# Kernel tuning notes

Measured on AMD Instinct MI355X. Metric: run time of the kernel, lower is better.

## Reference

```python
import jax, jax.numpy as jnp
import numpy as np

B, T, E, H, V = 64, 160, 512, 1024, 32000


def setup_inputs() -> dict:
    key = jax.random.key(0)
    ks = jax.random.split(key, 8)
    s = 1.0 / np.sqrt(H).astype(np.float32)
    return {
        "contexts": jax.random.randint(ks[0], (B, T), 0, V),
        "responses": jax.random.randint(ks[1], (B, T), 0, V),
        "emb": jax.random.normal(ks[2], (V, E), jnp.float32) * 0.02,
        "Wih": jax.random.uniform(ks[3], (4 * H, E), jnp.float32, -s, s),
        "Whh": jax.random.uniform(ks[4], (4 * H, H), jnp.float32, -s, s),
        "bih": jax.random.uniform(ks[5], (4 * H,), jnp.float32, -s, s),
        "bhh": jax.random.uniform(ks[6], (4 * H,), jnp.float32, -s, s),
        "M": jax.random.normal(ks[7], (H, H), jnp.float32),
    }


def _lstm_final_h(tokens, emb, Wih, Whh, bih, bhh):
    """Single-layer LSTM (PyTorch gate order i,f,g,o); returns final hidden state [B,H]."""
    x = emb[tokens]                      # [B, T, E]
    b = bih + bhh                        # [4H]
    hdim = Whh.shape[1]

    def step(carry, xt):
        h, c = carry
        gates = xt @ Wih.T + h @ Whh.T + b          # [B, 4H]
        i, f, g, o = jnp.split(gates, 4, axis=-1)
        c = jax.nn.sigmoid(f) * c + jax.nn.sigmoid(i) * jnp.tanh(g)
        h = jax.nn.sigmoid(o) * jnp.tanh(c)
        return (h, c), None

    h0 = jnp.zeros((tokens.shape[0], hdim), x.dtype)
    (h, _), _ = jax.lax.scan(step, (h0, h0), jnp.swapaxes(x, 0, 1))  # scan over time
    return h


def reference(contexts, responses, emb, Wih, Whh, bih, bhh, M):
    ch = _lstm_final_h(contexts, emb, Wih, Whh, bih, bhh)   # [B, H]
    rh = _lstm_final_h(responses, emb, Wih, Whh, bih, bhh)  # [B, H]
    # batched bilinear: sigmoid(diag(C @ M @ R^T)) -- replaces the per-example Python loop
    return jax.nn.sigmoid(jnp.einsum('bi,ij,bj->b', ch, M, rh))
```

## Files before the change

kernel.cpp:

```cpp
#include <hip/hip_runtime.h>
#include <math.h>


#define BB 64
#define TT 160
#define EE 512
#define HH 1024
#define G4 4096
#define ROWS 128
#define NBLK 64

typedef unsigned short u16;
typedef unsigned int u32;
typedef __attribute__((ext_vector_type(8))) __bf16 bf16x8;
typedef __attribute__((ext_vector_type(8))) short short8;
typedef __attribute__((ext_vector_type(4))) short short4v;
typedef __attribute__((ext_vector_type(4))) float f32x4;
typedef __attribute__((ext_vector_type(4))) u32 u32x4;
typedef __attribute__((ext_vector_type(2))) u32 u32x2;

__device__ __forceinline__ u16 f2b(float f) {
    unsigned u = __float_as_uint(f);
    u = u + 0x7fffu + ((u >> 16) & 1u);
    return (u16)(u >> 16);
}
__device__ __forceinline__ float b2f(u16 s) { return __uint_as_float(((unsigned)s) << 16); }

__device__ __forceinline__ f32x4 mfma16(short8 a, short8 b, f32x4 c) {
    return __builtin_amdgcn_mfma_f32_16x16x32_bf16(
        __builtin_bit_cast(bf16x8, a), __builtin_bit_cast(bf16x8, b), c, 0, 0, 0);
}

__device__ __forceinline__ void g2l16(const void* gsrc, void* ldst) {
    __builtin_amdgcn_global_load_lds(
        (const __attribute__((address_space(1))) u32*)gsrc,
        (__attribute__((address_space(3))) u32*)ldst, 16, 0, 0);
}
__device__ __forceinline__ void g2l16c(const void* gsrc, void* ldst) {
    __builtin_amdgcn_global_load_lds(
        (const __attribute__((address_space(1))) u32*)gsrc,
        (__attribute__((address_space(3))) u32*)ldst, 16, 0, 17);
}

__global__ __launch_bounds__(256) void cvt_kernel(const float* __restrict__ in,
                                                  u16* __restrict__ out, int n4) {
    int i = blockIdx.x * 256 + threadIdx.x;
    if (i < n4) {
        f32x4 v = *(const f32x4*)(in + (size_t)i * 4);
        short4v o;
        o.x = (short)f2b(v.x); o.y = (short)f2b(v.y);
        o.z = (short)f2b(v.z); o.w = (short)f2b(v.w);
        *(short4v*)(out + (size_t)i * 4) = o;
    }
}

__global__ __launch_bounds__(256) void pre_gemm2(
    const int* __restrict__ ctx, const int* __restrict__ rsp,
    const u16* __restrict__ embb, const u16* __restrict__ Wihb,
    const float* __restrict__ bih, const float* __restrict__ bhh,
    u16* __restrict__ xg)
{
    __shared__ __align__(16) u16 As[2][128][64];
    __shared__ __align__(16) u16 Ws[2][128][64];
    __shared__ int toks[128];
    const int tid = threadIdx.x;
    const int n0 = blockIdx.x * 128;
    const int t  = blockIdx.y;

    if (tid < 128) {
        int r = tid;
        toks[tid] = (r < BB) ? ctx[r * TT + t] : rsp[(r - BB) * TT + t];
    }
    __syncthreads();

    const u16* asrc[4]; const u16* bsrc[4];
    #pragma unroll
    for (int q = 0; q < 4; ++q) {
        int i = tid + q * 256;
        int row = i >> 3, c16 = i & 7;
        int scol = ((c16 ^ (row & 7)) * 8);
        asrc[q] = embb + (size_t)toks[row] * EE + scol;
        bsrc[q] = Wihb + (size_t)(n0 + row) * EE + scol;
    }

    const int lane = tid & 63, wave = tid >> 6;
    const int wr = (wave >> 1) * 64, wc = (wave & 1) * 64;
    const int l15 = lane & 15, l4 = lane >> 4;
    f32x4 acc[4][4] = {};

    #pragma unroll
    for (int q = 0; q < 4; ++q) {
        g2l16(asrc[q], (char*)&As[0][0][0] + (tid + q * 256) * 16);
        g2l16(bsrc[q], (char*)&Ws[0][0][0] + (tid + q * 256) * 16);
    }
    for (int it = 0; it < 8; ++it) {
        __syncthreads();
        if (it + 1 < 8) {
            int kk = (it + 1) * 64, bs = (it + 1) & 1;
            #pragma unroll
            for (int q = 0; q < 4; ++q) {
                g2l16(asrc[q] + kk, (char*)&As[bs][0][0] + (tid + q * 256) * 16);
                g2l16(bsrc[q] + kk, (char*)&Ws[bs][0][0] + (tid + q * 256) * 16);
            }
        }
        const int b = it & 1;
        #pragma unroll
        for (int ks = 0; ks < 2; ++ks) {
            int c16 = ks * 4 + l4;
            short8 a[4], w[4];
            #pragma unroll
            for (int mf = 0; mf < 4; ++mf) {
                int R = wr + mf * 16 + l15;
                a[mf] = *(const short8*)((const char*)&As[b][0][0] + R * 128 + ((c16 ^ (R & 7)) << 4));
            }
            #pragma unroll
            for (int nf = 0; nf < 4; ++nf) {
                int Nn = wc + nf * 16 + l15;
                w[nf] = *(const short8*)((const char*)&Ws[b][0][0] + Nn * 128 + ((c16 ^ (Nn & 7)) << 4));
            }
            #pragma unroll
            for (int mf = 0; mf < 4; ++mf)
                #pragma unroll
                for (int nf = 0; nf < 4; ++nf)
                    acc[mf][nf] = mfma16(a[mf], w[nf], acc[mf][nf]);
        }
    }

    u16* xp = xg + (size_t)t * ROWS * G4;
    #pragma unroll
    for (int nf = 0; nf < 4; ++nf) {
        int n = n0 + wc + nf * 16 + l15;
        float bias = bih[n] + bhh[n];
        #pragma unroll
        for (int mf = 0; mf < 4; ++mf)
            #pragma unroll
            for (int q = 0; q < 4; ++q) {
                int r = wr + mf * 16 + l4 * 4 + q;
                xp[(size_t)r * G4 + n] = f2b(acc[mf][nf][q] + bias);
            }
    }
}

__global__ __launch_bounds__(512, 2) void lstm_persist4(
    const u16* __restrict__ Whhb, const u16* __restrict__ xg,
    u16* __restrict__ hbuf, u32* __restrict__ flags)
{
    __shared__ __align__(16) u16 Abuf[64][512];
    __shared__ __align__(16) float G[2][64][132];

    const int tid = threadIdx.x;
    const int bx = blockIdx.x;
    const int cg = bx & 31, rg = bx >> 5;
    const int r0 = rg * 64, j0 = cg * 32;
    const int lane = tid & 63, w = tid >> 6;
    const int colt = w >> 2, q = w & 3;
    const int l15 = lane & 15, l4 = lane >> 4;

    short8 breg[4][8];
    #pragma unroll
    for (int nt = 0; nt < 4; ++nt) {
        int n = (colt * 2 + (nt >> 1)) * 1024 + j0 + (nt & 1) * 16 + l15;
        const u16* wp = Whhb + (size_t)n * HH + l4 * 8;
        #pragma unroll
        for (int z = 0; z < 8; ++z) {
            int kc = (z < 4) ? (q * 4 + z) : (16 + q * 4 + (z - 4));
            breg[nt][z] = *(const short8*)(wp + kc * 32);
        }
    }

    const int urow = tid >> 3;
    const int jj4  = (tid & 7) * 4;
    float cst[4] = {0.f, 0.f, 0.f, 0.f};

    __syncthreads();

    for (int t = 0; t < TT; ++t) {
        const u16* hin = hbuf + (size_t)(t & 1) * ROWS * HH;
        u16* hout      = hbuf + (size_t)((t + 1) & 1) * ROWS * HH;

        #pragma unroll
        for (int j = 0; j < 8; ++j) {
            int row = w * 8 + j;
            const u16* src = hin + (size_t)(r0 + row) * HH + ((lane ^ j) * 8);
            g2l16c(src, &Abuf[row][0]);
        }
        u32x2 xv[4];
        {
            const u16* xp = xg + ((size_t)t * ROWS + r0 + urow) * G4 + j0 + jj4;
            #pragma unroll
            for (int g = 0; g < 4; ++g)
                asm volatile("global_load_dwordx2 %0, %1, off"
                             : "=v"(xv[g]) : "v"(xp + g * HH));
        }

        f32x4 acc[4][4] = {};

        asm volatile("s_waitcnt vmcnt(4)" ::: "memory");
        __builtin_amdgcn_sched_barrier(0);
        __builtin_amdgcn_s_barrier();
        __builtin_amdgcn_sched_barrier(0);
        #pragma unroll
        for (int z4 = 0; z4 < 4; ++z4) {
            const int kcl = q * 4 + z4;
            short8 a[4];
            #pragma unroll
            for (int rt = 0; rt < 4; ++rt) {
                int row = rt * 16 + l15;
                int c16 = kcl * 4 + l4;
                a[rt] = *(const short8*)((const char*)&Abuf[0][0] +
                         row * 1024 + ((c16 ^ (l15 & 7)) << 4));
            }
            #pragma unroll
            for (int rt = 0; rt < 4; ++rt)
                #pragma unroll
                for (int nt = 0; nt < 4; ++nt)
                    acc[rt][nt] = mfma16(a[rt], breg[nt][z4], acc[rt][nt]);
        }
        asm volatile("s_waitcnt lgkmcnt(0)" ::: "memory");
        __builtin_amdgcn_s_barrier();
        __builtin_amdgcn_sched_barrier(0);

        #pragma unroll
        for (int j = 0; j < 8; ++j) {
            int row = w * 8 + j;
            const u16* src = hin + (size_t)(r0 + row) * HH + 512 + ((lane ^ j) * 8);
            g2l16c(src, &Abuf[row][0]);
        }
        asm volatile("s_waitcnt vmcnt(0)" ::: "memory");
        __builtin_amdgcn_sched_barrier(0);
        __builtin_amdgcn_s_barrier();
        __builtin_amdgcn_sched_barrier(0);
        #pragma unroll
        for (int z4 = 0; z4 < 4; ++z4) {
            const int kcl = q * 4 + z4;
            short8 a[4];
            #pragma unroll
            for (int rt = 0; rt < 4; ++rt) {
                int row = rt * 16 + l15;
                int c16 = kcl * 4 + l4;
                a[rt] = *(const short8*)((const char*)&Abuf[0][0] +
                         row * 1024 + ((c16 ^ (l15 & 7)) << 4));
            }
            #pragma unroll
            for (int rt = 0; rt < 4; ++rt)
                #pragma unroll
                for (int nt = 0; nt < 4; ++nt)
                    acc[rt][nt] = mfma16(a[rt], breg[nt][4 + z4], acc[rt][nt]);
        }

        if (q < 2) {
            #pragma unroll
            for (int rt = 0; rt < 4; ++rt)
                #pragma unroll
                for (int nt = 0; nt < 4; ++nt) {
                    int col = colt * 64 + nt * 16 + l15;
                    int rowb = rt * 16 + l4 * 4;
                    #pragma unroll
                    for (int e = 0; e < 4; ++e)
                        G[q][rowb + e][col] = acc[rt][nt][e];
                }
        }
        asm volatile("s_waitcnt lgkmcnt(0)" ::: "memory");
        __builtin_amdgcn_s_barrier();
        __builtin_amdgcn_sched_barrier(0);
        if (q >= 2) {
            #pragma unroll
            for (int rt = 0; rt < 4; ++rt)
                #pragma unroll
                for (int nt = 0; nt < 4; ++nt) {
                    int col = colt * 64 + nt * 16 + l15;
                    int rowb = rt * 16 + l4 * 4;
                    #pragma unroll
                    for (int e = 0; e < 4; ++e)
                        G[q - 2][rowb + e][col] += acc[rt][nt][e];
                }
        }
        asm volatile("s_waitcnt lgkmcnt(0)" ::: "memory");
        __builtin_amdgcn_s_barrier();
        __builtin_amdgcn_sched_barrier(0);

        float gv[4][4];
        #pragma unroll
        for (int g = 0; g < 4; ++g) {
            f32x4 a0 = *(const f32x4*)&G[0][urow][g * 32 + jj4];
            f32x4 a1 = *(const f32x4*)&G[1][urow][g * 32 + jj4];
            gv[g][0] = a0.x + a1.x + b2f((u16)(xv[g].x & 0xffffu));
            gv[g][1] = a0.y + a1.y + b2f((u16)(xv[g].x >> 16));
            gv[g][2] = a0.z + a1.z + b2f((u16)(xv[g].y & 0xffffu));
            gv[g][3] = a0.w + a1.w + b2f((u16)(xv[g].y >> 16));
        }
        u16 hp[4];
        #pragma unroll
        for (int e = 0; e < 4; ++e) {
            float ii = 1.f / (1.f + expf(-gv[0][e]));
            float ff = 1.f / (1.f + expf(-gv[1][e]));
            float gg = tanhf(gv[2][e]);
            float oo = 1.f / (1.f + expf(-gv[3][e]));
            cst[e] = ff * cst[e] + ii * gg;
            hp[e] = f2b(oo * tanhf(cst[e]));
        }
        u32x2 hw;
        hw.x = (u32)hp[0] | ((u32)hp[1] << 16);
        hw.y = (u32)hp[2] | ((u32)hp[3] << 16);
        {
            u16* hpt = hout + (size_t)(r0 + urow) * HH + j0 + jj4;
            asm volatile("global_store_dwordx2 %0, %1, off sc0 sc1"
                         :: "v"(hpt), "v"(hw) : "memory");
        }

        if (t < TT - 1) {
            asm volatile("s_waitcnt vmcnt(0)" ::: "memory");
            __builtin_amdgcn_s_barrier();
            __builtin_amdgcn_sched_barrier(0);
            const u32 target = (u32)(t + 1);
            if (tid == 0)
                asm volatile("global_store_dword %0, %1, off sc0 sc1"
                             :: "v"(flags + bx), "v"(target) : "memory");
            if (w == 0) {
                const u32* fp = flags + rg * 32 + (lane & 7) * 4;
                int spins = 0;
                while (true) {
                    u32x4 fv;
                    asm volatile("global_load_dwordx4 %0, %1, off sc0 sc1"
                                 : "=v"(fv) : "v"(fp));
                    asm volatile("s_waitcnt vmcnt(0)" ::: "memory");
                    bool ok = (fv.x >= target) & (fv.y >= target) &
                              (fv.z >= target) & (fv.w >= target);
                    if (__all(ok)) break;
                    __builtin_amdgcn_s_sleep(2);
                    if (++spins > 2000000) break;
                }
            }
            __builtin_amdgcn_s_barrier();
            __builtin_amdgcn_sched_barrier(0);
        }
    }
}

template<int MODE>
__global__ __launch_bounds__(256) void step_fused(
    const int* __restrict__ ctx, const int* __restrict__ rsp,
    const u16* __restrict__ embb, const u16* __restrict__ Wihb,
    const u16* __restrict__ Whhb, const u16* __restrict__ xg,
    const float* __restrict__ bih, const float* __restrict__ bhh,
    const u16* __restrict__ hin, u16* __restrict__ hout,
    float* __restrict__ c_ws, int t)
{
    __shared__ __align__(16) u16 As[2][64][64];
    __shared__ __align__(16) u16 Ws[2][32][64];
    __shared__ float gs[64][32];
    __shared__ int toks[64];

    const int tid = threadIdx.x;
    const int cg = blockIdx.x & 127, rg = blockIdx.x >> 7;
    const int r0 = rg * 64, j0 = cg * 8;

    if (MODE == 1) {
        if (tid < 64) {
            int r = r0 + tid;
            toks[tid] = (r < BB) ? ctx[r * TT + t] : rsp[(r - BB) * TT + t];
        }
        __syncthreads();
    }

    const int arow0 = tid >> 3, c16a = tid & 7;
    const int arow1 = arow0 + 32;
    const int acol0 = ((c16a ^ (arow0 & 7)) * 8);
    const int acol1 = ((c16a ^ (arow1 & 7)) * 8);
    const u16* hA0 = hin + (size_t)(r0 + arow0) * HH + acol0;
    const u16* hA1 = hin + (size_t)(r0 + arow1) * HH + acol1;
    const u16* eA0 = nullptr; const u16* eA1 = nullptr;
    if (MODE == 1) {
        eA0 = embb + (size_t)toks[arow0] * EE + acol0;
        eA1 = embb + (size_t)toks[arow1] * EE + acol1;
    }
    const int nn = tid >> 3, c16b = tid & 7;
    const int bcol = ((c16b ^ (nn & 7)) * 8);
    const int wrow = (nn >> 3) * HH + j0 + (nn & 7);
    const u16* wHh = Whhb + (size_t)wrow * HH + bcol;
    const u16* wIh = (MODE == 1) ? (Wihb + (size_t)wrow * EE + bcol) : nullptr;

    const int NK = (MODE == 1) ? 24 : 16;

    auto stage = [&](int bs, int it) {
        int kk = it * 64;
        const u16 *s0, *s1, *sw;
        if (MODE == 1 && kk < EE) {
            s0 = eA0 + kk; s1 = eA1 + kk; sw = wIh + kk;
        } else {
            int khh = (MODE == 1) ? kk - EE : kk;
            s0 = hA0 + khh; s1 = hA1 + khh; sw = wHh + khh;
        }
        g2l16(s0, (char*)&As[bs][0][0] + tid * 16);
        g2l16(s1, (char*)&As[bs][0][0] + (tid + 256) * 16);
        g2l16(sw, (char*)&Ws[bs][0][0] + tid * 16);
    };

    const int lane = tid & 63, wave = tid >> 6;
    const int wr = wave * 16;
    const int l15 = lane & 15, l4 = lane >> 4;
    f32x4 acc[2] = {};

    stage(0, 0);
    for (int it = 0; it < NK; ++it) {
        __syncthreads();
        if (it + 1 < NK) stage((it + 1) & 1, it + 1);
        const int b = it & 1;
        #pragma unroll
        for (int ks = 0; ks < 2; ++ks) {
            int c16 = ks * 4 + l4;
            int R = wr + l15;
            short8 a = *(const short8*)((const char*)&As[b][0][0] + R * 128 + ((c16 ^ (R & 7)) << 4));
            #pragma unroll
            for (int nf = 0; nf < 2; ++nf) {
                int Nn = nf * 16 + l15;
                short8 w = *(const short8*)((const char*)&Ws[b][0][0] + Nn * 128 + ((c16 ^ (Nn & 7)) << 4));
                acc[nf] = mfma16(a, w, acc[nf]);
            }
        }
    }
    __syncthreads();
    #pragma unroll
    for (int nf = 0; nf < 2; ++nf)
        #pragma unroll
        for (int q = 0; q < 4; ++q)
            gs[wr + l4 * 4 + q][nf * 16 + l15] = acc[nf][q];
    __syncthreads();

    const int e = tid * 2;
    const int row = e >> 3, jj = e & 7;
    const int rglob = r0 + row;
    float g0[4], g1[4];
    #pragma unroll
    for (int g = 0; g < 4; ++g) { g0[g] = gs[row][g * 8 + jj]; g1[g] = gs[row][g * 8 + jj + 1]; }
    if (MODE == 2) {
        const u16* xp = xg + ((size_t)t * ROWS + rglob) * G4 + j0 + jj;
        #pragma unroll
        for (int g = 0; g < 4; ++g) { g0[g] += b2f(xp[g * HH]); g1[g] += b2f(xp[g * HH + 1]); }
    } else {
        #pragma unroll
        for (int g = 0; g < 4; ++g) {
            int n = g * HH + j0 + jj;
            g0[g] += bih[n] + bhh[n];
            g1[g] += bih[n + 1] + bhh[n + 1];
        }
    }
    size_t cidx = ((size_t)blockIdx.x * 64 + row) * 8 + jj;
    float c0 = c_ws[cidx], c1 = c_ws[cidx + 1];
    float i0 = 1.f / (1.f + expf(-g0[0])), i1 = 1.f / (1.f + expf(-g1[0]));
    float f0 = 1.f / (1.f + expf(-g0[1])), f1 = 1.f / (1.f + expf(-g1[1]));
    float t0 = tanhf(g0[2]),               t1 = tanhf(g1[2]);
    float o0 = 1.f / (1.f + expf(-g0[3])), o1 = 1.f / (1.f + expf(-g1[3]));
    float cn0 = f0 * c0 + i0 * t0;
    float cn1 = f1 * c1 + i1 * t1;
    c_ws[cidx] = cn0; c_ws[cidx + 1] = cn1;
    float h0 = o0 * tanhf(cn0), h1 = o1 * tanhf(cn1);
    unsigned hpk = (unsigned)f2b(h0) | ((unsigned)f2b(h1) << 16);
    *(unsigned*)(hout + (size_t)rglob * HH + j0 + jj) = hpk;
}

__global__ __launch_bounds__(256) void step_gemm_f32(
    const int* __restrict__ ctx, const int* __restrict__ rsp,
    const float* __restrict__ emb, const float* __restrict__ Wih, const float* __restrict__ Whh,
    const u16* __restrict__ hb, float* __restrict__ gates, int t)
{
    __shared__ __align__(16) u16 As[64][32];
    __shared__ __align__(16) u16 Ws[64][32];
    __shared__ int toks[64];
    const int tid = threadIdx.x;
    const int n0 = blockIdx.x * 64;
    const int r0 = blockIdx.y * 64;
    const int part = blockIdx.z;
    if (tid < 64) {
        int r = r0 + tid;
        toks[tid] = (r < BB) ? ctx[r * TT + t] : rsp[(r - BB) * TT + t];
    }
    __syncthreads();
    const int lane = tid & 63, wave = tid >> 6;
    const int wr = (wave >> 1) * 32, wc = (wave & 1) * 32;
    const int l15 = lane & 15, l4 = lane >> 4;
    f32x4 acc[2][2] = {};
    const int kstart = part * 768;
    const int srow = tid >> 2;
    const int sseg = (tid & 3) * 8;
    for (int it = 0; it < 24; ++it) {
        const int kg = kstart + it * 32;
        const int kk = kg + sseg;
        if (kg < EE) {
            const float* s = emb + (size_t)toks[srow] * EE + kk;
            #pragma unroll
            for (int q = 0; q < 8; ++q) As[srow][sseg + q] = f2b(s[q]);
            const float* sw = Wih + (size_t)(n0 + srow) * EE + kk;
            #pragma unroll
            for (int q = 0; q < 8; ++q) Ws[srow][sseg + q] = f2b(sw[q]);
        } else {
            *(short8*)&As[srow][sseg] = *(const short8*)(hb + (size_t)(r0 + srow) * HH + (kk - EE));
            const float* sw = Whh + (size_t)(n0 + srow) * HH + (kk - EE);
            #pragma unroll
            for (int q = 0; q < 8; ++q) Ws[srow][sseg + q] = f2b(sw[q]);
        }
        __syncthreads();
        #pragma unroll
        for (int mf = 0; mf < 2; ++mf)
            #pragma unroll
            for (int nf = 0; nf < 2; ++nf)
                acc[mf][nf] = mfma16(*(const short8*)&As[wr + mf * 16 + l15][l4 * 8],
                                     *(const short8*)&Ws[wc + nf * 16 + l15][l4 * 8], acc[mf][nf]);
        __syncthreads();
    }
    float* gp = gates + (size_t)part * ROWS * G4;
    #pragma unroll
    for (int mf = 0; mf < 2; ++mf)
        #pragma unroll
        for (int nf = 0; nf < 2; ++nf)
            #pragma unroll
            for (int q = 0; q < 4; ++q) {
                int r = r0 + wr + mf * 16 + l4 * 4 + q;
                int n = n0 + wc + nf * 16 + l15;
                gp[(size_t)r * G4 + n] = acc[mf][nf][q];
            }
}

__global__ __launch_bounds__(256) void lstm_update0(
    const float* __restrict__ gates, const float* __restrict__ bih, const float* __restrict__ bhh,
    u16* __restrict__ hb, float* __restrict__ c)
{
    int idx = blockIdx.x * 256 + threadIdx.x;
    int r = idx >> 8;
    int jj = (idx & 255) * 4;
    const float* gp0 = gates + (size_t)r * G4;
    const float* gp1 = gates + (size_t)(ROWS + r) * G4;
    float gate[4][4];
    #pragma unroll
    for (int g = 0; g < 4; ++g) {
        int n = g * HH + jj;
        f32x4 a = *(const f32x4*)(gp0 + n);
        f32x4 b = *(const f32x4*)(gp1 + n);
        #pragma unroll
        for (int q = 0; q < 4; ++q) gate[g][q] = a[q] + b[q] + bih[n + q] + bhh[n + q];
    }
    int cidx = r * HH + jj;
    f32x4 cv = *(const f32x4*)(c + cidx);
    f32x4 cn; short4v hn;
    #pragma unroll
    for (int q = 0; q < 4; ++q) {
        float si = 1.f / (1.f + expf(-gate[0][q]));
        float sf = 1.f / (1.f + expf(-gate[1][q]));
        float tg = tanhf(gate[2][q]);
        float so = 1.f / (1.f + expf(-gate[3][q]));
        float cval = sf * cv[q] + si * tg;
        cn[q] = cval;
        ((short*)&hn)[q] = (short)f2b(so * tanhf(cval));
    }
    *(f32x4*)(c + cidx) = cn;
    *(short4v*)(hb + cidx) = hn;
}

__global__ __launch_bounds__(256) void bilinear(
    const u16* __restrict__ hb, const float* __restrict__ M, float* __restrict__ out)
{
    int b = blockIdx.x;
    __shared__ float chs[HH];
    __shared__ float red[256];
    const u16* ch = hb + (size_t)b * HH;
    const u16* rh = hb + (size_t)(BB + b) * HH;
    for (int i = threadIdx.x; i < HH; i += 256) chs[i] = b2f(ch[i]);
    __syncthreads();
    float vj[4] = {0.f, 0.f, 0.f, 0.f};
    for (int i = 0; i < HH; ++i) {
        float chi = chs[i];
        const float* Mr = M + (size_t)i * HH;
        #pragma unroll
        for (int q = 0; q < 4; ++q) vj[q] += chi * Mr[threadIdx.x + q * 256];
    }
    float acc = 0.f;
    #pragma unroll
    for (int q = 0; q < 4; ++q) acc += vj[q] * b2f(rh[threadIdx.x + q * 256]);
    red[threadIdx.x] = acc;
    __syncthreads();
    for (int s = 128; s > 0; s >>= 1) {
        if (threadIdx.x < s) red[threadIdx.x] += red[threadIdx.x + s];
        __syncthreads();
    }
    if (threadIdx.x == 0) out[b] = 1.0f / (1.0f + expf(-red[0]));
}

extern "C" void kernel_launch(void* const* d_in, const int* in_sizes, int n_in,
                              void* d_out, int out_size, void* d_ws, size_t ws_size,
                              hipStream_t stream) {
    const int*   ctx = (const int*)d_in[0];
    const int*   rsp = (const int*)d_in[1];
    const float* emb = (const float*)d_in[2];
    const float* Wih = (const float*)d_in[3];
    const float* Whh = (const float*)d_in[4];
    const float* bih = (const float*)d_in[5];
    const float* bhh = (const float*)d_in[6];
    const float* M   = (const float*)d_in[7];
    float* out = (float*)d_out;

    char* w = (char*)d_ws;
    u16*   hbuf  = (u16*)w;   w += (size_t)2 * ROWS * HH * 2;
    float* c_ws  = (float*)w; w += (size_t)ROWS * HH * 4;
    float* gates = (float*)w; w += (size_t)2 * ROWS * G4 * 4;
    u16*   embb  = (u16*)w;   w += (size_t)32000 * EE * 2;
    u16*   Wihb  = (u16*)w;   w += (size_t)G4 * EE * 2;
    u16*   Whhb  = (u16*)w;   w += (size_t)G4 * HH * 2;
    u32*   flags = (u32*)w;   w += 1024;
    size_t conv_need = (size_t)(w - (char*)d_ws);
    u16*   xg    = (u16*)w;   w += (size_t)TT * ROWS * G4 * 2;
    size_t xpre_need = (size_t)(w - (char*)d_ws);

    int mode = (ws_size >= xpre_need) ? 2 : (ws_size >= conv_need) ? 1 : 0;

    hipMemsetAsync(hbuf, 0, (size_t)2 * ROWS * HH * 2, stream);

    if (mode >= 1) {
        cvt_kernel<<<16000, 256, 0, stream>>>(emb, embb, 32000 * EE / 4);
        cvt_kernel<<<2048,  256, 0, stream>>>(Wih, Wihb, G4 * EE / 4);
        cvt_kernel<<<4096,  256, 0, stream>>>(Whh, Whhb, G4 * HH / 4);
    }

    if (mode == 2) {
        hipMemsetAsync(flags, 0, 1024, stream);
        pre_gemm2<<<dim3(G4 / 128, TT), 256, 0, stream>>>(ctx, rsp, embb, Wihb, bih, bhh, xg);
        lstm_persist4<<<NBLK, 512, 0, stream>>>(Whhb, xg, hbuf, flags);
        bilinear<<<BB, 256, 0, stream>>>(hbuf, M, out);
    } else if (mode == 1) {
        hipMemsetAsync(c_ws, 0, (size_t)ROWS * HH * 4, stream);
        for (int t = 0; t < TT; ++t) {
            const u16* hin = hbuf + (size_t)(t & 1) * ROWS * HH;
            u16* hout      = hbuf + (size_t)((t + 1) & 1) * ROWS * HH;
            step_fused<1><<<256, 256, 0, stream>>>(ctx, rsp, embb, Wihb, Whhb, xg,
                                                   bih, bhh, hin, hout, c_ws, t);
        }
        bilinear<<<BB, 256, 0, stream>>>(hbuf, M, out);
    } else {
        hipMemsetAsync(c_ws, 0, (size_t)ROWS * HH * 4, stream);
        u16* hb = hbuf;
        dim3 sg(G4 / 64, ROWS / 64, 2);
        for (int t = 0; t < TT; ++t) {
            step_gemm_f32<<<sg, 256, 0, stream>>>(ctx, rsp, emb, Wih, Whh, hb, gates, t);
            lstm_update0<<<128, 256, 0, stream>>>(gates, bih, bhh, hb, c_ws);
        }
        bilinear<<<BB, 256, 0, stream>>>(hb, M, out);
    }
}
```

Measured before the change: 2.005 ms.

## Load full hidden row into double LDS buffer, pad barrier flags, use fast activations

The persistent LSTM kernel now loads both halves of the hidden state into two LDS buffers in one pass and runs the full K loop without the mid-step reload and barrier. The gate-reduction buffer is aliased onto that LDS, which keeps shared memory near its old size. The inter-block flags are spread to one per 128-byte line, and the spin loop reads single dwords with a shorter sleep, to cut contention in the cross-block barrier. Sigmoid and tanh switch to exp2/rcp intrinsics, which lowers transcendental cost at a small accuracy risk.

```diff
diff --git a/kernel.cpp b/kernel.cpp
--- a/kernel.cpp
+++ b/kernel.cpp
@@ -16,7 +16,6 @@
 typedef __attribute__((ext_vector_type(8))) short short8;
 typedef __attribute__((ext_vector_type(4))) short short4v;
 typedef __attribute__((ext_vector_type(4))) float f32x4;
-typedef __attribute__((ext_vector_type(4))) u32 u32x4;
 typedef __attribute__((ext_vector_type(2))) u32 u32x2;
 
 __device__ __forceinline__ u16 f2b(float f) {
@@ -25,6 +24,14 @@
     return (u16)(u >> 16);
 }
 __device__ __forceinline__ float b2f(u16 s) { return __uint_as_float(((unsigned)s) << 16); }
+
+#define LOG2E 1.4426950408889634f
+__device__ __forceinline__ float sigf(float x) {
+    return __builtin_amdgcn_rcpf(1.f + __builtin_amdgcn_exp2f(-LOG2E * x));
+}
+__device__ __forceinline__ float tanhf_fast(float x) {
+    return 1.f - 2.f * __builtin_amdgcn_rcpf(1.f + __builtin_amdgcn_exp2f(2.f * LOG2E * x));
+}
 
 __device__ __forceinline__ f32x4 mfma16(short8 a, short8 b, f32x4 c) {
     return __builtin_amdgcn_mfma_f32_16x16x32_bf16(
@@ -141,12 +148,11 @@
     }
 }
 
-__global__ __launch_bounds__(512, 2) void lstm_persist4(
+__global__ __launch_bounds__(512, 2) void lstm_persist7(
     const u16* __restrict__ Whhb, const u16* __restrict__ xg,
-    u16* __restrict__ hbuf, u32* __restrict__ flags)
+    u16* __restrict__ hbuf, u32* __restrict__ barr)
 {
-    __shared__ __align__(16) u16 Abuf[64][512];
-    __shared__ __align__(16) float G[2][64][132];
+    __shared__ __align__(16) u16 Abuf[2][64][512];
 
     const int tid = threadIdx.x;
     const int bx = blockIdx.x;
@@ -156,6 +162,8 @@
     const int colt = w >> 2, q = w & 3;
     const int l15 = lane & 15, l4 = lane >> 4;
 
+    float* const G = (float*)&Abuf[0][0][0];
+
     short8 breg[4][8];
     #pragma unroll
     for (int nt = 0; nt < 4; ++nt) {
@@ -172,6 +180,8 @@
     const int jj4  = (tid & 7) * 4;
     float cst[4] = {0.f, 0.f, 0.f, 0.f};
 
+    u32* const cb = barr + (size_t)rg * 2048;
+
     __syncthreads();
 
     for (int t = 0; t < TT; ++t) {
@@ -181,8 +191,9 @@
         #pragma unroll
         for (int j = 0; j < 8; ++j) {
             int row = w * 8 + j;
-            const u16* src = hin + (size_t)(r0 + row) * HH + ((lane ^ j) * 8);
-            g2l16c(src, &Abuf[row][0]);
+            const u16* src = hin + (size_t)(r0 + row) * HH + ((lane ^ (row & 7)) * 8);
+            g2l16c(src,       &Abuf[0][row][0]);
+            g2l16c(src + 512, &Abuf[1][row][0]);
         }
         u32x2 xv[4];
         {
@@ -200,53 +211,28 @@
         __builtin_amdgcn_s_barrier();
         __builtin_amdgcn_sched_barrier(0);
         #pragma unroll
-        for (int z4 = 0; z4 < 4; ++z4) {
-            const int kcl = q * 4 + z4;
-            short8 a[4];
-            #pragma unroll
-            for (int rt = 0; rt < 4; ++rt) {
-                int row = rt * 16 + l15;
-                int c16 = kcl * 4 + l4;
-                a[rt] = *(const short8*)((const char*)&Abuf[0][0] +
-                         row * 1024 + ((c16 ^ (l15 & 7)) << 4));
-            }
-            #pragma unroll
-            for (int rt = 0; rt < 4; ++rt)
+        for (int half = 0; half < 2; ++half) {
+            #pragma unroll
+            for (int z4 = 0; z4 < 4; ++z4) {
+                const int kcl = q * 4 + z4;
+                short8 a[4];
                 #pragma unroll
-                for (int nt = 0; nt < 4; ++nt)
-                    acc[rt][nt] = mfma16(a[rt], breg[nt][z4], acc[rt][nt]);
+                for (int rt = 0; rt < 4; ++rt) {
+                    int row = rt * 16 + l15;
+                    int c16 = kcl * 4 + l4;
+                    a[rt] = *(const short8*)((const char*)&Abuf[half][0][0] +
+                             row * 1024 + ((c16 ^ (l15 & 7)) << 4));
+                }
+                #pragma unroll
+                for (int rt = 0; rt < 4; ++rt)
+                    #pragma unroll
+                    for (int nt = 0; nt < 4; ++nt)
+                        acc[rt][nt] = mfma16(a[rt], breg[nt][half * 4 + z4], acc[rt][nt]);
+            }
         }
         asm volatile("s_waitcnt lgkmcnt(0)" ::: "memory");
         __builtin_amdgcn_s_barrier();
         __builtin_amdgcn_sched_barrier(0);
-
-        #pragma unroll
-        for (int j = 0; j < 8; ++j) {
-            int row = w * 8 + j;
-            const u16* src = hin + (size_t)(r0 + row) * HH + 512 + ((lane ^ j) * 8);
-            g2l16c(src, &Abuf[row][0]);
-        }
-        asm volatile("s_waitcnt vmcnt(0)" ::: "memory");
-        __builtin_amdgcn_sched_barrier(0);
-        __builtin_amdgcn_s_barrier();
-        __builtin_amdgcn_sched_barrier(0);
-        #pragma unroll
-        for (int z4 = 0; z4 < 4; ++z4) {
-            const int kcl = q * 4 + z4;
-            short8 a[4];
-            #pragma unroll
-            for (int rt = 0; rt < 4; ++rt) {
-                int row = rt * 16 + l15;
-                int c16 = kcl * 4 + l4;
-                a[rt] = *(const short8*)((const char*)&Abuf[0][0] +
-                         row * 1024 + ((c16 ^ (l15 & 7)) << 4));
-            }
-            #pragma unroll
-            for (int rt = 0; rt < 4; ++rt)
-                #pragma unroll
-                for (int nt = 0; nt < 4; ++nt)
-                    acc[rt][nt] = mfma16(a[rt], breg[nt][4 + z4], acc[rt][nt]);
-        }
 
         if (q < 2) {
             #pragma unroll
@@ -257,7 +243,7 @@
                     int rowb = rt * 16 + l4 * 4;
                     #pragma unroll
                     for (int e = 0; e < 4; ++e)
-                        G[q][rowb + e][col] = acc[rt][nt][e];
+                        G[((size_t)q * 64 + rowb + e) * 132 + col] = acc[rt][nt][e];
                 }
         }
         asm volatile("s_waitcnt lgkmcnt(0)" ::: "memory");
@@ -272,18 +258,21 @@
                     int rowb = rt * 16 + l4 * 4;
                     #pragma unroll
                     for (int e = 0; e < 4; ++e)
-                        G[q - 2][rowb + e][col] += acc[rt][nt][e];
+                        G[((size_t)(q - 2) * 64 + rowb + e) * 132 + col] += acc[rt][nt][e];
                 }
         }
         asm volatile("s_waitcnt lgkmcnt(0)" ::: "memory");
         __builtin_amdgcn_s_barrier();
         __builtin_amdgcn_sched_barrier(0);
 
+        asm volatile("s_waitcnt vmcnt(0)" ::: "memory");
         float gv[4][4];
         #pragma unroll
         for (int g = 0; g < 4; ++g) {
-            f32x4 a0 = *(const f32x4*)&G[0][urow][g * 32 + jj4];
-            f32x4 a1 = *(const f32x4*)&G[1][urow][g * 32 + jj4];
+            const float* Gr0 = &G[((size_t)0 * 64 + urow) * 132 + g * 32 + jj4];
+            const float* Gr1 = &G[((size_t)1 * 64 + urow) * 132 + g * 32 + jj4];
+            f32x4 a0 = *(const f32x4*)Gr0;
+            f32x4 a1 = *(const f32x4*)Gr1;
             gv[g][0] = a0.x + a1.x + b2f((u16)(xv[g].x & 0xffffu));
             gv[g][1] = a0.y + a1.y + b2f((u16)(xv[g].x >> 16));
             gv[g][2] = a0.z + a1.z + b2f((u16)(xv[g].y & 0xffffu));
@@ -292,12 +281,12 @@
         u16 hp[4];
         #pragma unroll
         for (int e = 0; e < 4; ++e) {
-            float ii = 1.f / (1.f + expf(-gv[0][e]));
-            float ff = 1.f / (1.f + expf(-gv[1][e]));
-            float gg = tanhf(gv[2][e]);
-            float oo = 1.f / (1.f + expf(-gv[3][e]));
+            float ii = sigf(gv[0][e]);
+            float ff = sigf(gv[1][e]);
+            float gg = tanhf_fast(gv[2][e]);
+            float oo = sigf(gv[3][e]);
             cst[e] = ff * cst[e] + ii * gg;
-            hp[e] = f2b(oo * tanhf(cst[e]));
+            hp[e] = f2b(oo * tanhf_fast(cst[e]));
         }
         u32x2 hw;
         hw.x = (u32)hp[0] | ((u32)hp[1] << 16);
@@ -315,19 +304,17 @@
             const u32 target = (u32)(t + 1);
             if (tid == 0)
                 asm volatile("global_store_dword %0, %1, off sc0 sc1"
-                             :: "v"(flags + bx), "v"(target) : "memory");
+                             :: "v"(cb + cg * 32), "v"(target) : "memory");
             if (w == 0) {
-                const u32* fp = flags + rg * 32 + (lane & 7) * 4;
+                const u32* fp = cb + (lane & 31) * 32;
                 int spins = 0;
                 while (true) {
-                    u32x4 fv;
-                    asm volatile("global_load_dwordx4 %0, %1, off sc0 sc1"
-                                 : "=v"(fv) : "v"(fp));
+                    u32 v;
+                    asm volatile("global_load_dword %0, %1, off sc0 sc1"
+                                 : "=v"(v) : "v"(fp));
                     asm volatile("s_waitcnt vmcnt(0)" ::: "memory");
-                    bool ok = (fv.x >= target) & (fv.y >= target) &
-                              (fv.z >= target) & (fv.w >= target);
-                    if (__all(ok)) break;
-                    __builtin_amdgcn_s_sleep(2);
+                    if (__all(v >= target)) break;
+                    __builtin_amdgcn_s_sleep(1);
                     if (++spins > 2000000) break;
                 }
             }
@@ -605,7 +592,7 @@
     u16*   embb  = (u16*)w;   w += (size_t)32000 * EE * 2;
     u16*   Wihb  = (u16*)w;   w += (size_t)G4 * EE * 2;
     u16*   Whhb  = (u16*)w;   w += (size_t)G4 * HH * 2;
-    u32*   flags = (u32*)w;   w += 1024;
+    u32*   barr  = (u32*)w;   w += 16384;
     size_t conv_need = (size_t)(w - (char*)d_ws);
     u16*   xg    = (u16*)w;   w += (size_t)TT * ROWS * G4 * 2;
     size_t xpre_need = (size_t)(w - (char*)d_ws);
@@ -621,9 +608,9 @@
     }
 
     if (mode == 2) {
-        hipMemsetAsync(flags, 0, 1024, stream);
+        hipMemsetAsync(barr, 0, 16384, stream);
         pre_gemm2<<<dim3(G4 / 128, TT), 256, 0, stream>>>(ctx, rsp, embb, Wihb, bih, bhh, xg);
-        lstm_persist4<<<NBLK, 512, 0, stream>>>(Whhb, xg, hbuf, flags);
+        lstm_persist7<<<NBLK, 512, 0, stream>>>(Whhb, xg, hbuf, barr);
         bilinear<<<BB, 256, 0, stream>>>(hbuf, M, out);
     } else if (mode == 1) {
         hipMemsetAsync(c_ws, 0, (size_t)ROWS * HH * 4, stream);
```

Result: faster. 1.899 ms (median of 2 runs) (-5.3%).
